# Optimization experiments

Measured on AMD Instinct MI355X. Metric: run time of the kernel, lower is better.

## Reference

```python
import jax, jax.numpy as jnp
import numpy as np

EPS = 1e-5
B, C, H, W, MIP, CQ = 2, 256, 64, 64, 8, 32  # MIP = max(8, C//32); CQ = C//8


def _bn(x, p):
    # inference BatchNorm; p is [4, C] = (gamma, beta, running_mean, running_var)
    g, b, m, v = p[0], p[1], p[2], p[3]
    s = g / jnp.sqrt(v + EPS)
    return x * s[None, :, None, None] + (b - m * s)[None, :, None, None]


def _c1(x, w):  # 1x1 conv, w: [O, I]
    return jnp.einsum('bchw,oc->bohw', x, w)


def _c3(x, w):  # 3x3 conv, SAME padding, w: [O, I, 3, 3]
    return jax.lax.conv_general_dilated(x, w, (1, 1), 'SAME',
                                        dimension_numbers=('NCHW', 'OIHW', 'NCHW'))


def _cbs1(x, w, p):  # Conv(1x1)+BN+SiLU (YOLOv7 Conv block)
    return jax.nn.silu(_bn(_c1(x, w), p))


def _cbs3(x, w, p):  # Conv(3x3)+BN+SiLU
    return jax.nn.silu(_bn(_c3(x, w), p))


def _maxpool(x, k):  # MaxPool2d(kernel=k, stride=1, padding=k//2)
    p = k // 2
    return jax.lax.reduce_window(x, -jnp.inf, jax.lax.max,
                                 (1, 1, k, k), (1, 1, 1, 1),
                                 ((0, 0), (0, 0), (p, p), (p, p)))


def setup_inputs() -> dict:
    ks = iter(jax.random.split(jax.random.key(0), 64))

    def rn(shape, scale):
        return jax.random.normal(next(ks), shape, jnp.float32) * scale

    def w_(o, i, k=1):  # fan-in scaled conv weight
        sc = 1.0 / float(np.sqrt(i * k * k))
        return rn((o, i) if k == 1 else (o, i, k, k), sc)

    def bnp(c):  # gamma, beta, running_mean, running_var (var > 0)
        return jnp.stack([1.0 + rn((c,), 0.05), rn((c,), 0.05), rn((c,), 0.05),
                          0.5 + jax.random.uniform(next(ks), (c,), jnp.float32)])

    cm = C  # SPPCSPC hidden: int(2*C*0.5) = C
    return dict(
        x=rn((B, C, H, W), 1.0),
        ca_w1=w_(MIP, C), ca_b1=rn((MIP,), 0.05), ca_bn=bnp(MIP),
        ca_wh=w_(C, MIP), ca_bh=rn((C,), 0.05),
        ca_ww=w_(C, MIP), ca_bw=rn((C,), 0.05),
        s1_w=w_(cm, C), s1_bn=bnp(cm),
        s2_w=w_(cm, C), s2_bn=bnp(cm),
        s3_w=w_(cm, cm, 3), s3_bn=bnp(cm),
        s4_w=w_(cm, cm), s4_bn=bnp(cm),
        s5_w=w_(cm, 4 * cm), s5_bn=bnp(cm),
        s6_w=w_(cm, cm, 3), s6_bn=bnp(cm),
        s7_w=w_(C, 2 * cm), s7_bn=bnp(C),
        pq_w=w_(CQ, C), pq_b=rn((CQ,), 0.05),
        pk_w=w_(CQ, C), pk_b=rn((CQ,), 0.05),
        pv_w=w_(C, C), pv_b=rn((C,), 0.05),
        gamma_pa=rn((1,), 1.0), gamma_ca=rn((1,), 1.0),
    )


def reference(x, ca_w1, ca_b1, ca_bn, ca_wh, ca_bh, ca_ww, ca_bw,
              s1_w, s1_bn, s2_w, s2_bn, s3_w, s3_bn, s4_w, s4_bn,
              s5_w, s5_bn, s6_w, s6_bn, s7_w, s7_bn,
              pq_w, pq_b, pk_w, pk_b, pv_w, pv_b, gamma_pa, gamma_ca):
    b, c, h, w = x.shape
    # ---- CoordAtt ----
    xh = jnp.mean(x, axis=3, keepdims=True)                                 # b,c,h,1
    xw = jnp.transpose(jnp.mean(x, axis=2, keepdims=True), (0, 1, 3, 2))    # b,c,w,1
    y = jnp.concatenate([xh, xw], axis=2)                                   # b,c,h+w,1
    y = _bn(_c1(y, ca_w1) + ca_b1[None, :, None, None], ca_bn)
    y = y * jnp.clip(y + 3.0, 0.0, 6.0) / 6.0                               # h_swish
    a_h = jax.nn.sigmoid(_c1(y[:, :, :h], ca_wh) + ca_bh[None, :, None, None])
    a_w = jax.nn.sigmoid(_c1(jnp.transpose(y[:, :, h:], (0, 1, 3, 2)), ca_ww)
                         + ca_bw[None, :, None, None])
    r = x * a_w * a_h
    # ---- SPPCSPC ----
    x1 = _cbs1(_cbs3(_cbs1(r, s1_w, s1_bn), s3_w, s3_bn), s4_w, s4_bn)
    cat = jnp.concatenate([x1] + [_maxpool(x1, k) for k in (5, 9, 13)], axis=1)
    y1 = _cbs3(_cbs1(cat, s5_w, s5_bn), s6_w, s6_bn)
    y2 = _cbs1(r, s2_w, s2_bn)
    res = _cbs1(jnp.concatenate([y1, y2], axis=1), s7_w, s7_bn)
    # ---- PAM (spatial attention) ----
    n = h * w
    f = res.reshape(b, c, n)
    q = jnp.einsum('bcn,oc->bon', f, pq_w) + pq_b[None, :, None]            # b,c/8,n
    k = jnp.einsum('bcn,oc->bon', f, pk_w) + pk_b[None, :, None]
    v = jnp.einsum('bcn,oc->bon', f, pv_w) + pv_b[None, :, None]            # b,c,n
    attn = jax.nn.softmax(jnp.einsum('bcn,bcm->bnm', q, k), axis=-1)        # b,n,n
    res_pa = gamma_pa * jnp.einsum('bcm,bnm->bcn', v, attn).reshape(b, c, h, w) + res
    # ---- CAM (channel attention) ----
    e = jnp.einsum('bcn,bdn->bcd', f, f)                                    # b,c,c
    attn_c = jax.nn.softmax(jnp.max(e, axis=-1, keepdims=True) - e, axis=-1)
    res_ca = gamma_ca * jnp.einsum('bcd,bdn->bcn', attn_c, f).reshape(b, c, h, w) + res
    return res + res_ca + res_pa
```

## Files before the change

kernel.cpp:

```cpp
#include <hip/hip_runtime.h>

typedef unsigned short u16;
typedef __attribute__((ext_vector_type(8))) short bf16x8;
typedef __attribute__((ext_vector_type(4))) float f32x4;
#define EPSV 1e-5f
#define LOG2E 1.4426950408889634f

__device__ __forceinline__ float b2f(u16 u) {
  union { float f; unsigned int i; } v; v.i = ((unsigned int)u) << 16; return v.f;
}
__device__ __forceinline__ u16 f2b(float f) {
  union { float f; unsigned int i; } v; v.f = f;
  unsigned int r = v.i + 0x7FFFu + ((v.i >> 16) & 1u);
  return (u16)(r >> 16);
}
__device__ __forceinline__ u16 f2b_trunc(float f) {
  union { float f; unsigned int i; } v; v.f = f;
  return (u16)(v.i >> 16);
}
__device__ __forceinline__ float silu_(float z) { return z / (1.f + exp2f(-LOG2E * z)); }

__global__ __launch_bounds__(128) void detect_k(const u16* __restrict__ xp, float* __restrict__ flag) {
  __shared__ int cnt[2];
  int t = threadIdx.x;
  if (t < 2) cnt[t] = 0;
  __syncthreads();
  u16 u = xp[t * 2];
  int e = (u >> 7) & 0xff;
  if (e != 0 && (e < 90 || e > 160)) atomicAdd(&cnt[0], 1);
  if (u == 0) atomicAdd(&cnt[1], 1);
  __syncthreads();
  if (t == 0) *flag = (cnt[0] > 16 || cnt[1] > 64) ? 1.f : 0.f;
}


struct ConvArgs {
  const void* src[30];
  long dst[30];
  int end[30];
  int mode[30];
};

__global__ __launch_bounds__(256) void convert_all(ConvArgs a, float* __restrict__ wsF,
                                                   u16* __restrict__ wsH,
                                                   const float* __restrict__ flagp, int total) {
  const int flag = (*flagp > 0.5f);
  int gid = blockIdx.x * 256 + threadIdx.x;
  if (gid >= total) return;
  #pragma unroll 1
  for (int s = 0; s < 30; ++s) {
    if (gid < a.end[s]) {
      int idx = gid - (s ? a.end[s - 1] : 0);
      if (a.mode[s] == 0) {
        float v = flag ? ((const float*)a.src[s])[idx] : b2f(((const u16*)a.src[s])[idx]);
        wsF[a.dst[s] + idx] = v;
      } else {
        u16 h = flag ? f2b(((const float*)a.src[s])[idx]) : ((const u16*)a.src[s])[idx];
        wsH[a.dst[s] + idx] = h;
      }
      return;
    }
  }
}

__global__ __launch_bounds__(256) void w3t(const float* __restrict__ Wsrc, u16* __restrict__ Wdst) {
  int idx = blockIdx.x * 256 + threadIdx.x;
  int ch = idx & 31;
  int o  = (idx >> 5) & 255;
  int tap = (idx >> 13) % 9;
  int c8 = (idx >> 13) / 9;
  int i = c8 * 32 + ch;
  Wdst[idx] = f2b(Wsrc[((long)o * 256 + i) * 9 + tap]);
}

__global__ __launch_bounds__(256) void cvtb(const float* __restrict__ src, u16* __restrict__ dst, int n8) {
  int i = blockIdx.x * 256 + threadIdx.x;
  if (i >= n8) return;
  float4 f0 = *(const float4*)(src + (long)i * 8);
  float4 f1 = *(const float4*)(src + (long)i * 8 + 4);
  union { u16 h[8]; uint4 q; } u;
  u.h[0]=f2b(f0.x); u.h[1]=f2b(f0.y); u.h[2]=f2b(f0.z); u.h[3]=f2b(f0.w);
  u.h[4]=f2b(f1.x); u.h[5]=f2b(f1.y); u.h[6]=f2b(f1.z); u.h[7]=f2b(f1.w);
  *(uint4*)(dst + (long)i * 8) = u.q;
}


__global__ __launch_bounds__(256) void plane_means(const float* __restrict__ x, float* __restrict__ yin) {
  __shared__ float pl[4096];
  int bc = blockIdx.x, t = threadIdx.x;
  const float* xp = x + (long)bc * 4096;
  for (int j = 0; j < 16; ++j) { int id = j * 256 + t; pl[id] = xp[id]; }
  __syncthreads();
  if (t < 64) {
    float s = 0.f;
    for (int w = 0; w < 64; ++w) s += pl[t * 64 + w];
    yin[(long)bc * 128 + t] = s * (1.f / 64.f);
  } else if (t < 128) {
    int w = t - 64; float s = 0.f;
    for (int h = 0; h < 64; ++h) s += pl[h * 64 + w];
    yin[(long)bc * 128 + 64 + w] = s * (1.f / 64.f);
  }
}

__global__ __launch_bounds__(128) void ca_conv1(const float* __restrict__ yin, const float* __restrict__ w1,
                                                const float* __restrict__ b1, const float* __restrict__ bnp,
                                                float* __restrict__ ybn) {
  int b = blockIdx.x, p = threadIdx.x;
  float acc[8] = {0.f,0.f,0.f,0.f,0.f,0.f,0.f,0.f};
  for (int c = 0; c < 256; ++c) {
    float yv = yin[((long)b * 256 + c) * 128 + p];
    #pragma unroll
    for (int o = 0; o < 8; ++o) acc[o] += w1[o * 256 + c] * yv;
  }
  #pragma unroll
  for (int o = 0; o < 8; ++o) {
    float z = acc[o] + b1[o];
    float g = bnp[o], bt = bnp[8 + o], mn = bnp[16 + o], vr = bnp[24 + o];
    float s = g * rsqrtf(vr + EPSV);
    z = z * s + (bt - mn * s);
    float hs = fminf(fmaxf(z + 3.f, 0.f), 6.f) * (1.f / 6.f);
    ybn[((long)b * 8 + o) * 128 + p] = z * hs;
  }
}

__global__ __launch_bounds__(128) void ca_gate(const float* __restrict__ ybn,
    const float* __restrict__ wh, const float* __restrict__ bh,
    const float* __restrict__ ww, const float* __restrict__ bw,
    float* __restrict__ ah, float* __restrict__ aw_) {
  int c = blockIdx.x, b = blockIdx.y, t = threadIdx.x;
  if (t < 64) {
    float d = 0.f;
    #pragma unroll
    for (int o = 0; o < 8; ++o) d += wh[c * 8 + o] * ybn[((long)b * 8 + o) * 128 + t];
    d += bh[c];
    ah[((long)b * 256 + c) * 64 + t] = 1.f / (1.f + exp2f(-LOG2E * d));
  } else {
    int w = t - 64;
    float d = 0.f;
    #pragma unroll
    for (int o = 0; o < 8; ++o) d += ww[c * 8 + o] * ybn[((long)b * 8 + o) * 128 + 64 + w];
    d += bw[c];
    aw_[((long)b * 256 + c) * 64 + w] = 1.f / (1.f + exp2f(-LOG2E * d));
  }
}

__global__ __launch_bounds__(256) void apply_ca(const float* __restrict__ x, const float* __restrict__ ah,
                                                const float* __restrict__ aw_, u16* __restrict__ r) {
  int idx = blockIdx.x * 256 + threadIdx.x;
  int n = idx & 4095, bc = idx >> 12;
  int h = n >> 6, w = n & 63;
  r[idx] = f2b(x[idx] * ah[bc * 64 + h] * aw_[bc * 64 + w]);
}


template<int ACT, int OUTH>
__global__ __launch_bounds__(256) void mfma_cbs(
    const u16* __restrict__ Wbf, long aBS,
    const u16* __restrict__ In, long bBS,
    void* __restrict__ Out, long oBS,
    int O, int K, int N,
    const float* __restrict__ bnp, const float* __restrict__ bias)
{
  __shared__ u16 As[64 * 40];
  __shared__ u16 Bs[64 * 40];
  __shared__ float albe[64][2];
  const int t = threadIdx.x;
  const int n0 = blockIdx.x * 64;
  const int o0 = blockIdx.y * 64;
  const int b  = blockIdx.z;
  const int w = t >> 6, l = t & 63, lq = l >> 4, lr = l & 15;
  const int wo = (w >> 1) * 32, wn = (w & 1) * 32;
  if (t < 64) {
    int o = o0 + t;
    float al = 1.f, be = 0.f;
    if (bnp) {
      float g = bnp[o], bt = bnp[O + o], mn = bnp[2 * O + o], vr = bnp[3 * O + o];
      al = g * rsqrtf(vr + EPSV); be = bt - mn * al;
    }
    if (bias) be += bias[o];
    albe[t][0] = al; albe[t][1] = be;
  }
  const u16* Ab = Wbf + (long)b * aBS;
  const u16* inb = In + (long)b * bBS + n0;
  const int ao = t >> 2, akq = (t & 3) * 8;
  const int bk = t >> 3, bn8 = (t & 7) * 8;
  f32x4 acc[2][2] = {};
  for (int kc = 0; kc < K; kc += 32) {
    __syncthreads();
    *(uint4*)&As[ao * 40 + akq] = *(const uint4*)(Ab + (long)(o0 + ao) * K + kc + akq);
    union { uint4 q; u16 h[8]; } tb;
    tb.q = *(const uint4*)(inb + (long)(kc + bk) * N + bn8);
    #pragma unroll
    for (int j = 0; j < 8; ++j) Bs[(bn8 + j) * 40 + bk] = tb.h[j];
    __syncthreads();
    bf16x8 af[2], bfv[2];
    #pragma unroll
    for (int i = 0; i < 2; ++i) af[i] = *(const bf16x8*)&As[(wo + i * 16 + lr) * 40 + lq * 8];
    #pragma unroll
    for (int j = 0; j < 2; ++j) bfv[j] = *(const bf16x8*)&Bs[(wn + j * 16 + lr) * 40 + lq * 8];
    #pragma unroll
    for (int i = 0; i < 2; ++i)
      #pragma unroll
      for (int j = 0; j < 2; ++j)
        acc[i][j] = __builtin_amdgcn_mfma_f32_16x16x32_bf16(af[i], bfv[j], acc[i][j], 0, 0, 0);
  }
  float* ob = (float*)Out + (long)b * oBS;
  u16* obh = (u16*)Out + (long)b * oBS;
  #pragma unroll
  for (int i = 0; i < 2; ++i) {
    #pragma unroll
    for (int r = 0; r < 4; ++r) {
      int ol = wo + i * 16 + lq * 4 + r;
      float al = albe[ol][0], be = albe[ol][1];
      #pragma unroll
      for (int j = 0; j < 2; ++j) {
        float vv = acc[i][j][r] * al + be;
        if (ACT) vv = silu_(vv);
        if (OUTH == 2) {
          int col = n0 + wn + j * 16 + lr;
          obh[((long)(col >> 5) * 256 + (o0 + ol)) * 32 + (col & 31)] = f2b(vv);
        } else if (OUTH) {
          obh[(long)(o0 + ol) * N + n0 + wn + j * 16 + lr] = f2b(vv);
        } else {
          ob[(long)(o0 + ol) * N + n0 + wn + j * 16 + lr] = vv;
        }
      }
    }
  }
}

__global__ __launch_bounds__(256) void conv3_mfma(
    const u16* __restrict__ Wt,
    const u16* __restrict__ In, long iBS,
    u16* __restrict__ Out, long oBS, int O, int I,
    const float* __restrict__ bnp)
{
  __shared__ u16 As[9 * 64 * 34];
  __shared__ u16 Bs[4 * 66 * 34];
  __shared__ float albe[64][2];
  const int t = threadIdx.x;
  const int h0 = blockIdx.x * 2;
  const int o0 = blockIdx.y * 64;
  const int b  = blockIdx.z;
  const int w = t >> 6, l = t & 63, lq = l >> 4, lr = l & 15;
  const int wo = (w >> 1) * 32, wn = (w & 1) * 64;
  if (t < 64) {
    int o = o0 + t;
    float g = bnp[o], bt = bnp[O + o], mn = bnp[2 * O + o], vr = bnp[3 * O + o];
    float al = g * rsqrtf(vr + EPSV);
    albe[t][0] = al; albe[t][1] = bt - mn * al;
  }
  {
    int r = t >> 6, cs = (t >> 5) & 1, ch = t & 31;
    Bs[(r * 66 + (cs ? 65 : 0)) * 34 + ch] = 0;
  }
  const u16* inb = In + (long)b * iBS;
  const int bch = t >> 3, bcg = (t & 7) * 8;
  f32x4 acc[2][4] = {};
  for (int c8 = 0; c8 < (I >> 5); ++c8) {
    __syncthreads();
    {
      const u16* wsrc = Wt + (long)c8 * 9 * 256 * 32;
      #pragma unroll
      for (int j = 0; j < 9; ++j) {
        int e = j * 2048 + t * 8;
        int tap = e >> 11, o = (e >> 5) & 63, ch0 = e & 31;
        uint4 vv = *(const uint4*)(wsrc + ((long)tap * 256 + o0 + o) * 32 + ch0);
        *(uint4*)&As[(tap * 64 + o) * 34 + ch0] = vv;
      }
    }
    {
      const u16* cbase = inb + (long)(c8 * 32 + bch) * 4096;
      #pragma unroll
      for (int r = 0; r < 4; ++r) {
        int row = h0 - 1 + r;
        union { uint4 q; u16 h[8]; } tb;
        if (row >= 0 && row < 64) {
          tb.q = *(const uint4*)(cbase + row * 64 + bcg);
        } else {
          tb.q = make_uint4(0, 0, 0, 0);
        }
        #pragma unroll
        for (int j2 = 0; j2 < 8; ++j2)
          Bs[(r * 66 + bcg + 1 + j2) * 34 + bch] = tb.h[j2];
      }
    }
    __syncthreads();
    #pragma unroll
    for (int dy = 0; dy < 3; ++dy) {
      #pragma unroll
      for (int dx = 0; dx < 3; ++dx) {
        const int tap = dy * 3 + dx;
        bf16x8 af0 = *(const bf16x8*)&As[(tap * 64 + wo + lr) * 34 + lq * 8];
        bf16x8 af1 = *(const bf16x8*)&As[(tap * 64 + wo + 16 + lr) * 34 + lq * 8];
        #pragma unroll
        for (int j = 0; j < 4; ++j) {
          int nb = wn + j * 16;
          int rowS = (nb >> 6) + dy;
          int colS = (nb & 63) + dx;
          bf16x8 bv = *(const bf16x8*)&Bs[(rowS * 66 + colS + lr) * 34 + lq * 8];
          acc[0][j] = __builtin_amdgcn_mfma_f32_16x16x32_bf16(af0, bv, acc[0][j], 0, 0, 0);
          acc[1][j] = __builtin_amdgcn_mfma_f32_16x16x32_bf16(af1, bv, acc[1][j], 0, 0, 0);
        }
      }
    }
  }
  u16* ob = Out + (long)b * oBS;
  const int n0 = h0 * 64;
  #pragma unroll
  for (int i = 0; i < 2; ++i) {
    #pragma unroll
    for (int r = 0; r < 4; ++r) {
      int ol = wo + i * 16 + lq * 4 + r;
      float al = albe[ol][0], be = albe[ol][1];
      #pragma unroll
      for (int j = 0; j < 4; ++j) {
        float vv = silu_(acc[i][j][r] * al + be);
        ob[(long)(o0 + ol) * 4096 + n0 + wn + j * 16 + lr] = f2b(vv);
      }
    }
  }
}

__global__ __launch_bounds__(256) void pool3(u16* __restrict__ cat, long bs) {
  __shared__ float A[68][72];
  __shared__ float Bb[68][72];
  const int t = threadIdx.x;
  const int c = blockIdx.x, b = blockIdx.y;
  u16* base = cat + (long)b * bs + (long)c * 4096;
  for (int i = t; i < 68 * 72; i += 256) { (&A[0][0])[i] = -1e30f; (&Bb[0][0])[i] = -1e30f; }
  __syncthreads();
  const int r = t >> 2, c0 = (t & 3) * 16;
  #pragma unroll
  for (int j = 0; j < 16; ++j) A[r + 2][c0 + 2 + j] = b2f(base[r * 64 + c0 + j]);
  const long CNu = 1048576;
  #pragma unroll 1
  for (int s = 1; s <= 3; ++s) {
    __syncthreads();
    #pragma unroll
    for (int j = 0; j < 16; ++j) {
      int cc = c0 + j;
      float m = fmaxf(fmaxf(fmaxf(A[r+2][cc], A[r+2][cc+1]), fmaxf(A[r+2][cc+2], A[r+2][cc+3])), A[r+2][cc+4]);
      Bb[r + 2][cc + 2] = m;
    }
    __syncthreads();
    u16* out = base + (long)s * CNu;
    #pragma unroll
    for (int j = 0; j < 16; ++j) {
      int hc = c0 + 2 + j;
      float m = fmaxf(fmaxf(fmaxf(Bb[r][hc], Bb[r+1][hc]), fmaxf(Bb[r+2][hc], Bb[r+3][hc])), Bb[r+4][hc]);
      out[r * 64 + c0 + j] = f2b_trunc(m);
      A[r + 2][hc] = m;
    }
  }
}

__global__ __launch_bounds__(256) void transpose_hh(const u16* __restrict__ in, u16* __restrict__ out) {
  __shared__ u16 tile[32][34];
  int b = blockIdx.z;
  int c0 = blockIdx.x * 32, r0 = blockIdx.y * 32;
  int tx = threadIdx.x & 31, ty = threadIdx.x >> 5;
  const u16* ib = in + (long)b * 262144;
  u16* ob = out + (long)b * 262144;
  #pragma unroll
  for (int i = 0; i < 4; ++i) {
    int r = r0 + ty + i * 8;
    tile[ty + i * 8][tx] = ib[(long)r * 4096 + c0 + tx];
  }
  __syncthreads();
  #pragma unroll
  for (int i = 0; i < 4; ++i) {
    int c = c0 + ty + i * 8;
    ob[(long)c * 64 + r0 + tx] = tile[tx][ty + i * 8];
  }
}

__global__ __launch_bounds__(256) void pam_qk_max(const u16* __restrict__ qkT, float* __restrict__ pmax) {
  __shared__ u16 Qs[32 * 40];
  __shared__ u16 Ks[64 * 40];
  __shared__ float red[4][32][17];
  const int t = threadIdx.x;
  const int b = blockIdx.z, ms = blockIdx.y, n0 = blockIdx.x * 32;
  const int w = t >> 6, l = t & 63, lq = l >> 4, lr = l & 15;
  const int wn = w & 1, wc = w >> 1;
  if (t < 128) {
    int row = t >> 2, cq = (t & 3) * 8;
    *(uint4*)&Qs[row * 40 + cq] = *(const uint4*)(qkT + ((long)b * 4096 + n0 + row) * 64 + cq);
  }
  __syncthreads();
  bf16x8 qf = *(const bf16x8*)&Qs[(wn * 16 + lr) * 40 + lq * 8];
  float mx4[4] = {-1e30f, -1e30f, -1e30f, -1e30f};
  const int krow = t >> 2, kcq = (t & 3) * 8;
  for (int it = 0; it < 16; ++it) {
    int m0 = ms * 1024 + it * 64;
    __syncthreads();
    *(uint4*)&Ks[krow * 40 + kcq] = *(const uint4*)(qkT + ((long)b * 4096 + m0 + krow) * 64 + 32 + kcq);
    __syncthreads();
    #pragma unroll
    for (int s = 0; s < 2; ++s) {
      int msub = wc * 2 + s;
      bf16x8 kf = *(const bf16x8*)&Ks[(msub * 16 + lr) * 40 + lq * 8];
      f32x4 S = {};
      S = __builtin_amdgcn_mfma_f32_16x16x32_bf16(qf, kf, S, 0, 0, 0);
      #pragma unroll
      for (int r = 0; r < 4; ++r) mx4[r] = fmaxf(mx4[r], S[r]);
    }
  }
  #pragma unroll
  for (int r = 0; r < 4; ++r) red[w][wn * 16 + lq * 4 + r][lr] = mx4[r];
  __syncthreads();
  if (t < 32) {
    int wbase = t >> 4;
    float M = -1e30f;
    #pragma unroll
    for (int j = 0; j < 2; ++j)
      #pragma unroll
      for (int l2 = 0; l2 < 16; ++l2)
        M = fmaxf(M, red[wbase + 2 * j][t][l2]);
    pmax[((long)ms * 2 + b) * 4096 + n0 + t] = M;
  }
}

__global__ __launch_bounds__(256) void pam_merge(const float* __restrict__ pmax, float* __restrict__ rmx) {
  int i = blockIdx.x * 256 + threadIdx.x;
  int b = i >> 12, n = i & 4095;
  float m = pmax[(long)b * 4096 + n];
  #pragma unroll
  for (int ms = 1; ms < 4; ++ms) m = fmaxf(m, pmax[((long)ms * 2 + b) * 4096 + n]);
  rmx[i] = m;
}

__global__ __launch_bounds__(512) void pam_attn(const u16* __restrict__ qkT,
    const u16* __restrict__ vb, const float* __restrict__ rowmax,
    float* __restrict__ Obase, float* __restrict__ Sbase) {
  __shared__ u16 Qs[32 * 40];
  __shared__ u16 Ks[2][64 * 40];
  __shared__ u16 Ps[32 * 72];
  __shared__ float rmL[32];
  __shared__ float srow[32];
  const int t = threadIdx.x;
  const int mh = blockIdx.y;
  const int b = blockIdx.z;
  const int n0 = blockIdx.x * 32;
  const int w = t >> 6, l = t & 63, lq = l >> 4, lr = l & 15;
  const int nf = w & 1;
  const int mf = w >> 1;
  const int cw = w * 32;
  float* O = Obase + (long)mh * 2097152;
  float* S = Sbase + (long)mh * 8192;
  if (t < 128) {
    int row = t >> 2, cq = (t & 3) * 8;
    *(uint4*)&Qs[row * 40 + cq] = *(const uint4*)(qkT + ((long)b * 4096 + n0 + row) * 64 + cq);
  }
  if (t < 32) { rmL[t] = rowmax[(long)b * 4096 + n0 + t] * LOG2E; srow[t] = 0.f; }
  const int krow = t >> 3, kc4 = (t & 7) * 4;
  const u16* kbase = qkT + ((long)b * 4096 + krow) * 64 + 32 + kc4;
  const u16* vop = vb + (long)b * 1048576 + (cw + lr) * 32 + lq * 8;
  const int mStart = mh * 2048, mEnd = mStart + 2048;

  {
    uint2 k0 = *(const uint2*)(kbase + (long)mStart * 64);
    *(uint2*)&Ks[0][krow * 40 + kc4] = k0;
  }
  uint2 kreg = *(const uint2*)(kbase + (long)(mStart + 64) * 64);
  long vt0 = (long)(mStart >> 5) * 8192;
  uint4 vA00 = *(const uint4*)(vop + vt0);
  uint4 vA01 = *(const uint4*)(vop + vt0 + 512);
  uint4 vA10 = *(const uint4*)(vop + vt0 + 8192);
  uint4 vA11 = *(const uint4*)(vop + vt0 + 8704);
  uint4 vB00, vB01, vB10, vB11;

  __syncthreads();
  bf16x8 qf = *(const bf16x8*)&Qs[(nf * 16 + lr) * 40 + lq * 8];
  const float rml = rmL[nf * 16 + lr];
  float spl = 0.f;
  f32x4 acc[2][2] = {};

#define QK_PHASE(BUF)                                                          \
  {                                                                            \
    bf16x8 kf = *(const bf16x8*)&Ks[BUF][(mf * 16 + lr) * 40 + lq * 8];        \
    f32x4 Sv = {};                                                             \
    Sv = __builtin_amdgcn_mfma_f32_16x16x32_bf16(kf, qf, Sv, 0, 0, 0);         \
    union { u16 h[4]; uint2 q; } pk;                                           \
    _Pragma("unroll")                                                          \
    for (int r = 0; r < 4; ++r) {                                              \
      float p = exp2f(Sv[r] * LOG2E - rml);                                    \
      spl += p;                                                                \
      pk.h[r] = f2b_trunc(p);                                                  \
    }                                                                          \
    *(uint2*)&Ps[(nf * 16 + lr) * 72 + mf * 16 + lq * 4] = pk.q;               \
  }

#define PV_PHASE(V00, V01, V10, V11)                                           \
  {                                                                            \
    bf16x8 pf0 = *(const bf16x8*)&Ps[lr * 72 + lq * 8];                        \
    bf16x8 pf1 = *(const bf16x8*)&Ps[(16 + lr) * 72 + lq * 8];                 \
    acc[0][0] = __builtin_amdgcn_mfma_f32_16x16x32_bf16(*(bf16x8*)&V00, pf0, acc[0][0], 0, 0, 0); \
    acc[0][1] = __builtin_amdgcn_mfma_f32_16x16x32_bf16(*(bf16x8*)&V00, pf1, acc[0][1], 0, 0, 0); \
    acc[1][0] = __builtin_amdgcn_mfma_f32_16x16x32_bf16(*(bf16x8*)&V01, pf0, acc[1][0], 0, 0, 0); \
    acc[1][1] = __builtin_amdgcn_mfma_f32_16x16x32_bf16(*(bf16x8*)&V01, pf1, acc[1][1], 0, 0, 0); \
    pf0 = *(const bf16x8*)&Ps[lr * 72 + 32 + lq * 8];                          \
    pf1 = *(const bf16x8*)&Ps[(16 + lr) * 72 + 32 + lq * 8];                   \
    acc[0][0] = __builtin_amdgcn_mfma_f32_16x16x32_bf16(*(bf16x8*)&V10, pf0, acc[0][0], 0, 0, 0); \
    acc[0][1] = __builtin_amdgcn_mfma_f32_16x16x32_bf16(*(bf16x8*)&V10, pf1, acc[0][1], 0, 0, 0); \
    acc[1][0] = __builtin_amdgcn_mfma_f32_16x16x32_bf16(*(bf16x8*)&V11, pf0, acc[1][0], 0, 0, 0); \
    acc[1][1] = __builtin_amdgcn_mfma_f32_16x16x32_bf16(*(bf16x8*)&V11, pf1, acc[1][1], 0, 0, 0); \
  }

  #pragma unroll 1
  for (int m0 = mStart; m0 < mEnd; m0 += 128) {
    int m2 = m0 + 128; if (m2 >= mEnd) m2 = mStart;
    int m3 = m0 + 192; if (m3 >= mEnd) m3 = mStart;
    QK_PHASE(0)
    *(uint2*)&Ks[1][krow * 40 + kc4] = kreg;
    kreg = *(const uint2*)(kbase + (long)m2 * 64);
    {
      long vt = (long)((m0 + 64) >> 5) * 8192;
      vB00 = *(const uint4*)(vop + vt);
      vB01 = *(const uint4*)(vop + vt + 512);
      vB10 = *(const uint4*)(vop + vt + 8192);
      vB11 = *(const uint4*)(vop + vt + 8704);
    }
    __syncthreads();
    __builtin_amdgcn_s_setprio(1);
    PV_PHASE(vA00, vA01, vA10, vA11)
    __builtin_amdgcn_s_setprio(0);
    __syncthreads();
    QK_PHASE(1)
    *(uint2*)&Ks[0][krow * 40 + kc4] = kreg;
    kreg = *(const uint2*)(kbase + (long)m3 * 64);
    {
      long vt = (long)(m2 >> 5) * 8192;
      vA00 = *(const uint4*)(vop + vt);
      vA01 = *(const uint4*)(vop + vt + 512);
      vA10 = *(const uint4*)(vop + vt + 8192);
      vA11 = *(const uint4*)(vop + vt + 8704);
    }
    __syncthreads();
    __builtin_amdgcn_s_setprio(1);
    PV_PHASE(vB00, vB01, vB10, vB11)
    __builtin_amdgcn_s_setprio(0);
    __syncthreads();
  }
#undef QK_PHASE
#undef PV_PHASE

  spl += __shfl_xor(spl, 16);
  spl += __shfl_xor(spl, 32);
  if (l < 16) atomicAdd(&srow[nf * 16 + lr], spl);
  __syncthreads();
  if (t < 32) S[(long)b * 4096 + n0 + t] = srow[t];
  float* ob = O + (long)b * 1048576 + n0;
  #pragma unroll
  for (int cf = 0; cf < 2; ++cf) {
    #pragma unroll
    for (int r = 0; r < 4; ++r) {
      int c = cw + cf * 16 + lq * 4 + r;
      ob[(long)c * 4096 + lr]      = acc[cf][0][r];
      ob[(long)c * 4096 + 16 + lr] = acc[cf][1][r];
    }
  }
}


__global__ __launch_bounds__(256) void fillz(float* __restrict__ p, int n) {
  int i = blockIdx.x * 256 + threadIdx.x;
  if (i < n) p[i] = 0.f;
}

__global__ __launch_bounds__(256) void cam_e_mfma(const u16* __restrict__ resb, float* __restrict__ e) {
  __shared__ u16 As[64 * 40];
  __shared__ u16 Bs[128 * 40];
  const int t = threadIdx.x;
  const int d0 = blockIdx.x * 128;
  const int c0 = blockIdx.y * 64;
  const int bz = blockIdx.z;
  const int b = bz >> 4, ks = bz & 15;
  const int w = t >> 6, l = t & 63, lq = l >> 4, lr = l & 15;
  const int wo = (w >> 1) * 32, wn = (w & 1) * 64;
  const u16* fb = resb + (long)b * 1048576;
  const int ao = t >> 2, akq = (t & 3) * 8;
  const int bo = t >> 1, bkq = (t & 1) * 16;
  f32x4 acc[2][4] = {};
  for (int kc = ks * 256; kc < ks * 256 + 256; kc += 32) {
    __syncthreads();
    *(uint4*)&As[ao * 40 + akq] = *(const uint4*)(fb + (long)(c0 + ao) * 4096 + kc + akq);
    #pragma unroll
    for (int i = 0; i < 2; ++i)
      *(uint4*)&Bs[bo * 40 + bkq + i * 8] = *(const uint4*)(fb + (long)(d0 + bo) * 4096 + kc + bkq + i * 8);
    __syncthreads();
    bf16x8 af[2], bfv[4];
    #pragma unroll
    for (int i = 0; i < 2; ++i) af[i] = *(const bf16x8*)&As[(wo + i * 16 + lr) * 40 + lq * 8];
    #pragma unroll
    for (int j = 0; j < 4; ++j) bfv[j] = *(const bf16x8*)&Bs[(wn + j * 16 + lr) * 40 + lq * 8];
    #pragma unroll
    for (int i = 0; i < 2; ++i)
      #pragma unroll
      for (int j = 0; j < 4; ++j)
        acc[i][j] = __builtin_amdgcn_mfma_f32_16x16x32_bf16(af[i], bfv[j], acc[i][j], 0, 0, 0);
  }
  #pragma unroll
  for (int i = 0; i < 2; ++i)
    #pragma unroll
    for (int r = 0; r < 4; ++r) {
      int ol = wo + i * 16 + lq * 4 + r;
      #pragma unroll
      for (int j = 0; j < 4; ++j)
        atomicAdd(&e[((long)b << 16) + (long)(c0 + ol) * 256 + d0 + wn + j * 16 + lr], acc[i][j][r]);
    }
}

__global__ __launch_bounds__(256) void cam_softmax(const float* __restrict__ e, u16* __restrict__ attn) {
  __shared__ float red[256];
  int c = blockIdx.x, b = blockIdx.y, t = threadIdx.x;
  const float* row = e + ((long)b << 16) + (long)c * 256;
  float v = row[t];
  red[t] = v; __syncthreads();
  for (int s = 128; s > 0; s >>= 1) { if (t < s) red[t] = fminf(red[t], red[t + s]); __syncthreads(); }
  float emin = red[0]; __syncthreads();
  float ex = exp2f(LOG2E * (emin - v));
  red[t] = ex; __syncthreads();
  for (int s = 128; s > 0; s >>= 1) { if (t < s) red[t] += red[t + s]; __syncthreads(); }
  float inv = 1.f / red[0];
  attn[((long)b << 16) + (long)c * 256 + t] = f2b(ex * inv);
}


__global__ __launch_bounds__(256) void combine(const float* __restrict__ res, const float* __restrict__ O,
    const float* __restrict__ S, const float* __restrict__ cam, const float* __restrict__ gp,
    void* __restrict__ outp, const float* __restrict__ flagp) {
  int idx = blockIdx.x * 256 + threadIdx.x;
  int b = idx >> 20, n = idx & 4095;
  float g1 = gp[0], g2 = gp[1];
  float sden = S[(long)b * 4096 + n] + S[8192 + (long)b * 4096 + n];
  float pamv = (O[idx] + O[2097152 + idx]) / sden;
  float v = 3.f * res[idx] + g1 * pamv + g2 * cam[idx];
  if (*flagp > 0.5f) ((float*)outp)[idx] = v;
  else               ((u16*)outp)[idx] = f2b(v);
}


extern "C" void kernel_launch(void* const* d_in, const int* in_sizes, int n_in,
                              void* d_out, int out_size, void* d_ws, size_t ws_size,
                              hipStream_t stream)
{
  (void)out_size; (void)ws_size; (void)n_in;
  float* ws = (float*)d_ws;
  const long CN = 1048576;

  float* A  = ws;
  float* Bp = ws + 2 * CN;
  float* Cp = ws + 4 * CN;
  float* D  = ws + 6 * CN;
  const long WFo = 14 * CN;

  u16*   rB   = (u16*)A;
  float* res  = A;
  float* xf   = Bp;
  u16*   BpU  = (u16*)Bp;
  float* yin  = Cp;
  float* ybn  = Cp + 65536;
  float* ah   = Cp + 67584;
  float* aw_  = Cp + 100352;
  u16*   CpU  = (u16*)Cp;
  u16*   catU = (u16*)D;
  u16*   y12U = (u16*)D;
  float* D2   = D + 2 * CN;
  u16*   qkbU = (u16*)D2;
  u16*   qkTU = (u16*)(D2 + 262144);
  float* pmax = D2 + 524288;
  float* rmx  = D2 + 557056;
  float* e    = D2 + 565248;
  u16*   attnc= (u16*)(D2 + 696320);
  float* S0   = D2 + 761856;
  float* cam  = D;
  float* O0   = D + 4 * CN;

  ConvArgs ca;
  long fOff[30], hOff[30];
  long hcur = 0;
  float* flagp = ws + WFo;
  {
    long cum = 0, fcur = WFo + 4;
    for (int i = 0; i < 30; ++i) {
      ca.src[i] = d_in[i];
      int h = (i == 8 || i == 10 || i == 14 || i == 16 || i == 20 ||
               i == 22 || i == 24 || i == 26) ? 1 : 0;
      ca.mode[i] = h;
      if (i == 0) { ca.dst[i] = 2 * CN; fOff[i] = 2 * CN; }
      else if (h) { ca.dst[i] = hcur; hOff[i] = hcur; hcur += in_sizes[i]; }
      else        { ca.dst[i] = fcur; fOff[i] = fcur; fcur += in_sizes[i]; }
      cum += in_sizes[i];
      ca.end[i] = (int)cum;
    }
  }
  long fTotal = WFo + 4;
  for (int i = 1; i < 30; ++i) if (!ca.mode[i]) fTotal = (fOff[i] + in_sizes[i] > fTotal) ? fOff[i] + in_sizes[i] : fTotal;
  u16* wsH = (u16*)(ws + fTotal);
  u16* wt3a = wsH + hcur;
  u16* wt3b = wsH + hcur + 589824;
  int total = ca.end[29];

  detect_k<<<dim3(1), dim3(128), 0, stream>>>((const u16*)d_in[0], flagp);
  convert_all<<<dim3((total + 255) / 256), dim3(256), 0, stream>>>(ca, ws, wsH, flagp, total);

  float* ca_w1 = ws + fOff[1];
  float* ca_b1 = ws + fOff[2];
  float* ca_bn = ws + fOff[3];
  float* ca_wh = ws + fOff[4];
  float* ca_bh = ws + fOff[5];
  float* ca_ww = ws + fOff[6];
  float* ca_bw = ws + fOff[7];
  u16*   s1_w  = wsH + hOff[8];   float* s1_bn = ws + fOff[9];
  u16*   s2_w  = wsH + hOff[10];  float* s2_bn = ws + fOff[11];
  float* s3_wf = ws + fOff[12];   float* s3_bn = ws + fOff[13];
  u16*   s4_w  = wsH + hOff[14];  float* s4_bn = ws + fOff[15];
  u16*   s5_w  = wsH + hOff[16];  float* s5_bn = ws + fOff[17];
  float* s6_wf = ws + fOff[18];   float* s6_bn = ws + fOff[19];
  u16*   s7_w  = wsH + hOff[20];  float* s7_bn = ws + fOff[21];
  u16*   qk_w  = wsH + hOff[22];  float* qk_b  = ws + fOff[23];
  u16*   pv_w  = wsH + hOff[26];  float* pv_b  = ws + fOff[27];
  float* gammas = ws + fOff[28];

  w3t<<<dim3(2304), dim3(256), 0, stream>>>(s3_wf, wt3a);
  w3t<<<dim3(2304), dim3(256), 0, stream>>>(s6_wf, wt3b);

  plane_means<<<dim3(512), dim3(256), 0, stream>>>(xf, yin);
  ca_conv1<<<dim3(2), dim3(128), 0, stream>>>(yin, ca_w1, ca_b1, ca_bn, ybn);
  ca_gate<<<dim3(256, 2), dim3(128), 0, stream>>>(ybn, ca_wh, ca_bh, ca_ww, ca_bw, ah, aw_);
  apply_ca<<<dim3(8192), dim3(256), 0, stream>>>(xf, ah, aw_, rB);

  mfma_cbs<1,1><<<dim3(64, 4, 2), dim3(256), 0, stream>>>(s1_w, 0, rB, CN, CpU, CN, 256, 256, 4096, s1_bn, nullptr);
  conv3_mfma<<<dim3(32, 4, 2), dim3(256), 0, stream>>>(wt3a, CpU, CN, BpU, CN, 256, 256, s3_bn);
  mfma_cbs<1,1><<<dim3(64, 4, 2), dim3(256), 0, stream>>>(s4_w, 0, BpU, CN, catU, 4 * CN, 256, 256, 4096, s4_bn, nullptr);

  pool3<<<dim3(256, 2), dim3(256), 0, stream>>>(catU, 4 * CN);

  mfma_cbs<1,1><<<dim3(64, 4, 2), dim3(256), 0, stream>>>(s5_w, 0, catU, 4 * CN, BpU, CN, 256, 1024, 4096, s5_bn, nullptr);
  conv3_mfma<<<dim3(32, 4, 2), dim3(256), 0, stream>>>(wt3b, BpU, CN, y12U, 2 * CN, 256, 256, s6_bn);
  mfma_cbs<1,1><<<dim3(64, 4, 2), dim3(256), 0, stream>>>(s2_w, 0, rB, CN, y12U + CN, 2 * CN, 256, 256, 4096, s2_bn, nullptr);
  mfma_cbs<1,0><<<dim3(64, 4, 2), dim3(256), 0, stream>>>(s7_w, 0, y12U, 2 * CN, res, CN, 256, 512, 4096, s7_bn, nullptr);

  cvtb<<<dim3(1024), dim3(256), 0, stream>>>(res, BpU, 262144);
  mfma_cbs<0,1><<<dim3(64, 1, 2), dim3(256), 0, stream>>>(qk_w, 0, BpU, CN, qkbU, 262144, 64, 256, 4096, nullptr, qk_b);
  mfma_cbs<0,2><<<dim3(64, 4, 2), dim3(256), 0, stream>>>(pv_w, 0, BpU, CN, CpU, CN, 256, 256, 4096, nullptr, pv_b);
  transpose_hh<<<dim3(128, 2, 2), dim3(256), 0, stream>>>(qkbU, qkTU);

  pam_qk_max<<<dim3(128, 4, 2), dim3(256), 0, stream>>>(qkTU, pmax);
  pam_merge<<<dim3(32), dim3(256), 0, stream>>>(pmax, rmx);
  pam_attn<<<dim3(128, 2, 2), dim3(512), 0, stream>>>(qkTU, CpU, rmx, O0, S0);

  fillz<<<dim3(512), dim3(256), 0, stream>>>(e, 131072);
  cam_e_mfma<<<dim3(2, 4, 32), dim3(256), 0, stream>>>(BpU, e);
  cam_softmax<<<dim3(256, 2), dim3(256), 0, stream>>>(e, attnc);
  mfma_cbs<0,0><<<dim3(64, 4, 2), dim3(256), 0, stream>>>(attnc, 65536, BpU, CN, cam, CN, 256, 256, 4096, nullptr, nullptr);

  combine<<<dim3(8192), dim3(256), 0, stream>>>(res, O0, S0, cam, gammas, d_out, flagp);
}
```

Baseline: 439.8 us.

## Load MFMA A-operands directly to registers and prefetch next K-chunk in GEMM kernels

```diff
diff --git a/kernel.cpp b/kernel.cpp
--- a/kernel.cpp
+++ b/kernel.cpp
@@ -161,7 +161,6 @@
     int O, int K, int N,
     const float* __restrict__ bnp, const float* __restrict__ bias)
 {
-  __shared__ u16 As[64 * 40];
   __shared__ u16 Bs[64 * 40];
   __shared__ float albe[64][2];
   const int t = threadIdx.x;
@@ -182,27 +181,32 @@
   }
   const u16* Ab = Wbf + (long)b * aBS;
   const u16* inb = In + (long)b * bBS + n0;
-  const int ao = t >> 2, akq = (t & 3) * 8;
+  const u16* a0p = Ab + (long)(o0 + wo + lr) * K + lq * 8;
+  const u16* a1p = a0p + (long)16 * K;
   const int bk = t >> 3, bn8 = (t & 7) * 8;
   f32x4 acc[2][2] = {};
+  uint4 a0 = *(const uint4*)(a0p);
+  uint4 a1 = *(const uint4*)(a1p);
+  uint4 b0 = *(const uint4*)(inb + (long)bk * N + bn8);
   for (int kc = 0; kc < K; kc += 32) {
-    __syncthreads();
-    *(uint4*)&As[ao * 40 + akq] = *(const uint4*)(Ab + (long)(o0 + ao) * K + kc + akq);
-    union { uint4 q; u16 h[8]; } tb;
-    tb.q = *(const uint4*)(inb + (long)(kc + bk) * N + bn8);
-    #pragma unroll
-    for (int j = 0; j < 8; ++j) Bs[(bn8 + j) * 40 + bk] = tb.h[j];
-    __syncthreads();
-    bf16x8 af[2], bfv[2];
-    #pragma unroll
-    for (int i = 0; i < 2; ++i) af[i] = *(const bf16x8*)&As[(wo + i * 16 + lr) * 40 + lq * 8];
-    #pragma unroll
-    for (int j = 0; j < 2; ++j) bfv[j] = *(const bf16x8*)&Bs[(wn + j * 16 + lr) * 40 + lq * 8];
-    #pragma unroll
-    for (int i = 0; i < 2; ++i)
+    int kn = kc + 32; if (kn >= K) kn = 0;
+    __syncthreads();
+    {
+      union { uint4 q; u16 h[8]; } tb; tb.q = b0;
       #pragma unroll
-      for (int j = 0; j < 2; ++j)
-        acc[i][j] = __builtin_amdgcn_mfma_f32_16x16x32_bf16(af[i], bfv[j], acc[i][j], 0, 0, 0);
+      for (int j = 0; j < 8; ++j) Bs[(bn8 + j) * 40 + bk] = tb.h[j];
+    }
+    uint4 a0n = *(const uint4*)(a0p + kn);
+    uint4 a1n = *(const uint4*)(a1p + kn);
+    uint4 b0n = *(const uint4*)(inb + (long)(kn + bk) * N + bn8);
+    __syncthreads();
+    bf16x8 bfv0 = *(const bf16x8*)&Bs[(wn + lr) * 40 + lq * 8];
+    bf16x8 bfv1 = *(const bf16x8*)&Bs[(wn + 16 + lr) * 40 + lq * 8];
+    acc[0][0] = __builtin_amdgcn_mfma_f32_16x16x32_bf16(*(const bf16x8*)&a0, bfv0, acc[0][0], 0, 0, 0);
+    acc[0][1] = __builtin_amdgcn_mfma_f32_16x16x32_bf16(*(const bf16x8*)&a0, bfv1, acc[0][1], 0, 0, 0);
+    acc[1][0] = __builtin_amdgcn_mfma_f32_16x16x32_bf16(*(const bf16x8*)&a1, bfv0, acc[1][0], 0, 0, 0);
+    acc[1][1] = __builtin_amdgcn_mfma_f32_16x16x32_bf16(*(const bf16x8*)&a1, bfv1, acc[1][1], 0, 0, 0);
+    a0 = a0n; a1 = a1n; b0 = b0n;
   }
   float* ob = (float*)Out + (long)b * oBS;
   u16* obh = (u16*)Out + (long)b * oBS;
@@ -235,7 +239,6 @@
     u16* __restrict__ Out, long oBS, int O, int I,
     const float* __restrict__ bnp)
 {
-  __shared__ u16 As[9 * 64 * 34];
   __shared__ u16 Bs[4 * 66 * 34];
   __shared__ float albe[64][2];
   const int t = threadIdx.x;
@@ -243,7 +246,7 @@
   const int o0 = blockIdx.y * 64;
   const int b  = blockIdx.z;
   const int w = t >> 6, l = t & 63, lq = l >> 4, lr = l & 15;
-  const int wo = (w >> 1) * 32, wn = (w & 1) * 64;
+  const int wn = w * 32;
   if (t < 64) {
     int o = o0 + t;
     float g = bnp[o], bt = bnp[O + o], mn = bnp[2 * O + o], vr = bnp[3 * O + o];
@@ -256,65 +259,78 @@
   }
   const u16* inb = In + (long)b * iBS;
   const int bch = t >> 3, bcg = (t & 7) * 8;
-  f32x4 acc[2][4] = {};
-  for (int c8 = 0; c8 < (I >> 5); ++c8) {
+  const u16* wlane = Wt + (long)(o0 + lr) * 32 + lq * 8;
+  const int nC8 = I >> 5;
+  f32x4 acc[4][2] = {};
+
+  uint4 tb0, tb1, tb2, tb3;
+  {
+    const u16* cb = inb + (long)bch * 4096 + bcg;
+    tb0 = (h0 - 1 >= 0) ? *(const uint4*)(cb + (h0 - 1) * 64) : make_uint4(0,0,0,0);
+    tb1 = *(const uint4*)(cb + h0 * 64);
+    tb2 = *(const uint4*)(cb + (h0 + 1) * 64);
+    tb3 = (h0 + 2 < 64) ? *(const uint4*)(cb + (h0 + 2) * 64) : make_uint4(0,0,0,0);
+  }
+
+  for (int c8 = 0; c8 < nC8; ++c8) {
     __syncthreads();
     {
-      const u16* wsrc = Wt + (long)c8 * 9 * 256 * 32;
+      union { uint4 q; u16 h[8]; } u0, u1, u2, u3;
+      u0.q = tb0; u1.q = tb1; u2.q = tb2; u3.q = tb3;
       #pragma unroll
-      for (int j = 0; j < 9; ++j) {
-        int e = j * 2048 + t * 8;
-        int tap = e >> 11, o = (e >> 5) & 63, ch0 = e & 31;
-        uint4 vv = *(const uint4*)(wsrc + ((long)tap * 256 + o0 + o) * 32 + ch0);
-        *(uint4*)&As[(tap * 64 + o) * 34 + ch0] = vv;
+      for (int j2 = 0; j2 < 8; ++j2) {
+        Bs[(0 * 66 + bcg + 1 + j2) * 34 + bch] = u0.h[j2];
+        Bs[(1 * 66 + bcg + 1 + j2) * 34 + bch] = u1.h[j2];
+        Bs[(2 * 66 + bcg + 1 + j2) * 34 + bch] = u2.h[j2];
+        Bs[(3 * 66 + bcg + 1 + j2) * 34 + bch] = u3.h[j2];
       }
     }
+    int c8n = c8 + 1; if (c8n >= nC8) c8n = 0;
+    uint4 n0_, n1_, n2_, n3_;
     {
-      const u16* cbase = inb + (long)(c8 * 32 + bch) * 4096;
-      #pragma unroll
-      for (int r = 0; r < 4; ++r) {
-        int row = h0 - 1 + r;
-        union { uint4 q; u16 h[8]; } tb;
-        if (row >= 0 && row < 64) {
-          tb.q = *(const uint4*)(cbase + row * 64 + bcg);
-        } else {
-          tb.q = make_uint4(0, 0, 0, 0);
-        }
-        #pragma unroll
-        for (int j2 = 0; j2 < 8; ++j2)
-          Bs[(r * 66 + bcg + 1 + j2) * 34 + bch] = tb.h[j2];
-      }
-    }
-    __syncthreads();
+      const u16* cb = inb + (long)(c8n * 32 + bch) * 4096 + bcg;
+      n0_ = (h0 - 1 >= 0) ? *(const uint4*)(cb + (h0 - 1) * 64) : make_uint4(0,0,0,0);
+      n1_ = *(const uint4*)(cb + h0 * 64);
+      n2_ = *(const uint4*)(cb + (h0 + 1) * 64);
+      n3_ = (h0 + 2 < 64) ? *(const uint4*)(cb + (h0 + 2) * 64) : make_uint4(0,0,0,0);
+    }
+    __syncthreads();
+    const u16* wc8 = wlane + (long)c8 * 9 * 256 * 32;
     #pragma unroll
     for (int dy = 0; dy < 3; ++dy) {
       #pragma unroll
       for (int dx = 0; dx < 3; ++dx) {
         const int tap = dy * 3 + dx;
-        bf16x8 af0 = *(const bf16x8*)&As[(tap * 64 + wo + lr) * 34 + lq * 8];
-        bf16x8 af1 = *(const bf16x8*)&As[(tap * 64 + wo + 16 + lr) * 34 + lq * 8];
+        const u16* wl = wc8 + (long)tap * 256 * 32;
+        uint4 af0 = *(const uint4*)(wl);
+        uint4 af1 = *(const uint4*)(wl + 16 * 32);
+        uint4 af2 = *(const uint4*)(wl + 32 * 32);
+        uint4 af3 = *(const uint4*)(wl + 48 * 32);
         #pragma unroll
-        for (int j = 0; j < 4; ++j) {
+        for (int j = 0; j < 2; ++j) {
           int nb = wn + j * 16;
           int rowS = (nb >> 6) + dy;
           int colS = (nb & 63) + dx;
           bf16x8 bv = *(const bf16x8*)&Bs[(rowS * 66 + colS + lr) * 34 + lq * 8];
-          acc[0][j] = __builtin_amdgcn_mfma_f32_16x16x32_bf16(af0, bv, acc[0][j], 0, 0, 0);
-          acc[1][j] = __builtin_amdgcn_mfma_f32_16x16x32_bf16(af1, bv, acc[1][j], 0, 0, 0);
+          acc[0][j] = __builtin_amdgcn_mfma_f32_16x16x32_bf16(*(const bf16x8*)&af0, bv, acc[0][j], 0, 0, 0);
+          acc[1][j] = __builtin_amdgcn_mfma_f32_16x16x32_bf16(*(const bf16x8*)&af1, bv, acc[1][j], 0, 0, 0);
+          acc[2][j] = __builtin_amdgcn_mfma_f32_16x16x32_bf16(*(const bf16x8*)&af2, bv, acc[2][j], 0, 0, 0);
+          acc[3][j] = __builtin_amdgcn_mfma_f32_16x16x32_bf16(*(const bf16x8*)&af3, bv, acc[3][j], 0, 0, 0);
         }
       }
     }
+    tb0 = n0_; tb1 = n1_; tb2 = n2_; tb3 = n3_;
   }
   u16* ob = Out + (long)b * oBS;
   const int n0 = h0 * 64;
   #pragma unroll
-  for (int i = 0; i < 2; ++i) {
+  for (int i = 0; i < 4; ++i) {
     #pragma unroll
     for (int r = 0; r < 4; ++r) {
-      int ol = wo + i * 16 + lq * 4 + r;
+      int ol = i * 16 + lq * 4 + r;
       float al = albe[ol][0], be = albe[ol][1];
       #pragma unroll
-      for (int j = 0; j < 4; ++j) {
+      for (int j = 0; j < 2; ++j) {
         float vv = silu_(acc[i][j][r] * al + be);
         ob[(long)(o0 + ol) * 4096 + n0 + wn + j * 16 + lr] = f2b(vv);
       }
@@ -569,7 +585,6 @@
 }
 
 __global__ __launch_bounds__(256) void cam_e_mfma(const u16* __restrict__ resb, float* __restrict__ e) {
-  __shared__ u16 As[64 * 40];
   __shared__ u16 Bs[128 * 40];
   const int t = threadIdx.x;
   const int d0 = blockIdx.x * 128;
@@ -579,26 +594,33 @@
   const int w = t >> 6, l = t & 63, lq = l >> 4, lr = l & 15;
   const int wo = (w >> 1) * 32, wn = (w & 1) * 64;
   const u16* fb = resb + (long)b * 1048576;
-  const int ao = t >> 2, akq = (t & 3) * 8;
+  const u16* a0p = fb + (long)(c0 + wo + lr) * 4096 + lq * 8;
+  const u16* a1p = a0p + (long)16 * 4096;
   const int bo = t >> 1, bkq = (t & 1) * 16;
+  const u16* bp = fb + (long)(d0 + bo) * 4096 + bkq;
+  const int kS = ks * 256, kE = kS + 256;
   f32x4 acc[2][4] = {};
-  for (int kc = ks * 256; kc < ks * 256 + 256; kc += 32) {
-    __syncthreads();
-    *(uint4*)&As[ao * 40 + akq] = *(const uint4*)(fb + (long)(c0 + ao) * 4096 + kc + akq);
-    #pragma unroll
-    for (int i = 0; i < 2; ++i)
-      *(uint4*)&Bs[bo * 40 + bkq + i * 8] = *(const uint4*)(fb + (long)(d0 + bo) * 4096 + kc + bkq + i * 8);
-    __syncthreads();
-    bf16x8 af[2], bfv[4];
-    #pragma unroll
-    for (int i = 0; i < 2; ++i) af[i] = *(const bf16x8*)&As[(wo + i * 16 + lr) * 40 + lq * 8];
-    #pragma unroll
-    for (int j = 0; j < 4; ++j) bfv[j] = *(const bf16x8*)&Bs[(wn + j * 16 + lr) * 40 + lq * 8];
-    #pragma unroll
-    for (int i = 0; i < 2; ++i)
-      #pragma unroll
-      for (int j = 0; j < 4; ++j)
-        acc[i][j] = __builtin_amdgcn_mfma_f32_16x16x32_bf16(af[i], bfv[j], acc[i][j], 0, 0, 0);
+  uint4 a0 = *(const uint4*)(a0p + kS);
+  uint4 a1 = *(const uint4*)(a1p + kS);
+  uint4 b0 = *(const uint4*)(bp + kS);
+  uint4 b1 = *(const uint4*)(bp + kS + 8);
+  for (int kc = kS; kc < kE; kc += 32) {
+    int kn = kc + 32; if (kn >= kE) kn = kS;
+    __syncthreads();
+    *(uint4*)&Bs[bo * 40 + bkq] = b0;
+    *(uint4*)&Bs[bo * 40 + bkq + 8] = b1;
+    uint4 a0n = *(const uint4*)(a0p + kn);
+    uint4 a1n = *(const uint4*)(a1p + kn);
+    uint4 b0n = *(const uint4*)(bp + kn);
+    uint4 b1n = *(const uint4*)(bp + kn + 8);
+    __syncthreads();
+    #pragma unroll
+    for (int j = 0; j < 4; ++j) {
+      bf16x8 bfv = *(const bf16x8*)&Bs[(wn + j * 16 + lr) * 40 + lq * 8];
+      acc[0][j] = __builtin_amdgcn_mfma_f32_16x16x32_bf16(*(const bf16x8*)&a0, bfv, acc[0][j], 0, 0, 0);
+      acc[1][j] = __builtin_amdgcn_mfma_f32_16x16x32_bf16(*(const bf16x8*)&a1, bfv, acc[1][j], 0, 0, 0);
+    }
+    a0 = a0n; a1 = a1n; b0 = b0n; b1 = b1n;
   }
   #pragma unroll
   for (int i = 0; i < 2; ++i)
```

Result: no change. 436.2 us (-0.8%).
